# Kernel optimization log

Hardware: AMD Instinct MI355X
Metric: run time of the kernel (lower is better)

The kernel has to match this reference:

```python
import jax, jax.numpy as jnp
import numpy as np

N_SAMPLE = 32
BETA = 1.0


def setup_inputs() -> dict:
    key = jax.random.key(0)
    k1, k2 = jax.random.split(key)
    # small scales so the gaussian kernel over 512 dims does not underflow
    x = jax.random.normal(k1, (2048, 512), dtype=jnp.float32) * 0.05
    W = jax.random.normal(k2, (512, 2048), dtype=jnp.float32) * 0.02  # Dense kernel [in, hidden]
    return {"x": x, "W": W}


def reference(x, W):
    B, H = x.shape[0], W.shape[1]
    # Encoder: h = x W ; z = softmax(h * beita)
    h = x @ W                                   # [B, H]
    z = jax.nn.softmax(h * BETA, axis=-1)       # [B, H]
    # Sampler: tf.random.categorical treats z (probs) as LOGITS -> same here.
    key = jax.random.key(42)
    # tf gives [B, n_sample]; jax categorical with shape=(NS, B) then .T matches that,
    # and the original code then RESHAPES (not transposes) to [NS, B] -> replicate scramble.
    samp = jax.random.categorical(key, z, axis=-1, shape=(N_SAMPLE, B)).T  # [B, NS]
    samp = samp.reshape(N_SAMPLE, B)            # faithful reshape, not transpose
    onehot = jax.nn.one_hot(samp, H, dtype=x.dtype)          # [NS, B, H]
    # tensordot(onehot, W, axes=[2,1]) -> gather rows of W^T as dense matmul
    x_decoded = jnp.einsum('nbh,dh->nbd', onehot, W)          # [NS, B, D]
    # gauss(x[None], x_decoded), var=1
    diff = x[None, :, :] - x_decoded                          # [NS, B, D]
    coeff = 1.0 / jnp.sqrt(2.0 * jnp.pi)
    temp = coeff * jnp.exp(-0.5 * jnp.sum(diff * diff, axis=-1))  # [NS, B]
    weight = temp / jnp.mean(temp, axis=0)                    # broadcast over NS
    return (h, z, onehot, x_decoded, weight)
```

## Files before the change

### kernel.cpp

```cpp
#include <hip/hip_runtime.h>
#include <stdint.h>
#include <math.h>

static constexpr int BDIM = 2048;
static constexpr int HDIM = 2048;
static constexpr int DDIM = 512;
static constexpr int NSAMP = 32;

static constexpr size_t OFF_H  = 0;
static constexpr size_t OFF_Z  = (size_t)BDIM * HDIM;
static constexpr size_t OFF_OH = OFF_Z + (size_t)BDIM * HDIM;
static constexpr size_t OFF_XD = OFF_OH + (size_t)NSAMP * BDIM * HDIM;
static constexpr size_t OFF_W  = OFF_XD + (size_t)NSAMP * BDIM * DDIM;

static constexpr size_t WS_WT    = 0;
static constexpr size_t WS_XB    = 1048576;
static constexpr size_t WS_WTB   = WS_XB + 524288;
static constexpr size_t WS_SAMP  = WS_WTB + 524288;
static constexpr size_t WS_TEMP  = WS_SAMP + 65536;
static constexpr size_t WS_DELTA = WS_TEMP + 65536;

typedef __attribute__((ext_vector_type(8))) short short8;
typedef __attribute__((ext_vector_type(4))) float f32x4;

__device__ __forceinline__ ushort f2bf(float f) {
  uint32_t x = __float_as_uint(f);
  return (ushort)((x + 0x7FFFu + ((x >> 16) & 1u)) >> 16);
}

__global__ __launch_bounds__(256) void cast_x_kernel(const float* __restrict__ x,
                                                     ushort* __restrict__ xb) {
  const int i = (blockIdx.x * 256 + threadIdx.x) * 4;
  float4 v = *(const float4*)(x + i);
  ushort4 o = {f2bf(v.x), f2bf(v.y), f2bf(v.z), f2bf(v.w)};
  *(ushort4*)(xb + i) = o;
}

__global__ __launch_bounds__(256) void transpose_kernel(const float* __restrict__ W,
                                                        float* __restrict__ Wt,
                                                        ushort* __restrict__ Wtb) {
  __shared__ float tile[32][33];
  const int tx = threadIdx.x & 31, ty = threadIdx.x >> 5;
  const int bx = blockIdx.x;
  const int by = blockIdx.y;
#pragma unroll
  for (int i = 0; i < 32; i += 8)
    tile[ty + i][tx] = W[(size_t)(by * 32 + ty + i) * HDIM + bx * 32 + tx];
  __syncthreads();
#pragma unroll
  for (int i = 0; i < 32; i += 8) {
    float v = tile[tx][ty + i];
    const size_t o = (size_t)(bx * 32 + ty + i) * DDIM + by * 32 + tx;
    Wt[o] = v;
    Wtb[o] = f2bf(v);
  }
}

__global__ __launch_bounds__(256) void gemm_mfma_kernel(const ushort* __restrict__ xb,
                                                        const ushort* __restrict__ wtb,
                                                        float* __restrict__ h) {
  __shared__ short As[128][72];
  __shared__ short Bs[128][72];
  const int tid = threadIdx.x;
  const int bm = blockIdx.y * 128, bn = blockIdx.x * 128;
  const int wave = tid >> 6, lane = tid & 63;
  const int wm = (wave >> 1) * 64, wn = (wave & 1) * 64;
  const int lrow = lane & 15, lk = (lane >> 4) * 8;

  f32x4 acc[4][4] = {};

  const int srow = tid >> 3;
  const int scol = (tid & 7) * 8;

  for (int k0 = 0; k0 < DDIM; k0 += 64) {
#pragma unroll
    for (int p = 0; p < 4; ++p) {
      const int r = srow + p * 32;
      short8 av = *(const short8*)(xb + (size_t)(bm + r) * DDIM + k0 + scol);
      short8 bv = *(const short8*)(wtb + (size_t)(bn + r) * DDIM + k0 + scol);
      *(short8*)&As[r][scol] = av;
      *(short8*)&Bs[r][scol] = bv;
    }
    __syncthreads();
#pragma unroll
    for (int kk = 0; kk < 64; kk += 32) {
      short8 af[4], bf[4];
#pragma unroll
      for (int i = 0; i < 4; ++i) {
        af[i] = *(const short8*)&As[wm + i * 16 + lrow][kk + lk];
        bf[i] = *(const short8*)&Bs[wn + i * 16 + lrow][kk + lk];
      }
#pragma unroll
      for (int i = 0; i < 4; ++i)
#pragma unroll
        for (int j = 0; j < 4; ++j)
          acc[i][j] = __builtin_amdgcn_mfma_f32_16x16x32_bf16(af[i], bf[j], acc[i][j], 0, 0, 0);
    }
    __syncthreads();
  }
#pragma unroll
  for (int i = 0; i < 4; ++i)
#pragma unroll
    for (int j = 0; j < 4; ++j)
#pragma unroll
      for (int rg = 0; rg < 4; ++rg) {
        const int row = bm + wm + i * 16 + (lane >> 4) * 4 + rg;
        const int col = bn + wn + j * 16 + (lane & 15);
        h[(size_t)row * HDIM + col] = acc[i][j][rg];
      }
}

__global__ __launch_bounds__(256) void softmax_kernel(const float* __restrict__ h,
                                                      float* __restrict__ z,
                                                      float* __restrict__ rowDelta) {
  const int b = blockIdx.x;
  const int tid = threadIdx.x;
  const int lane = tid & 63, wav = tid >> 6;
  const float* row = h + (size_t)b * HDIM;
  float* zrow = z + (size_t)b * HDIM;
  __shared__ float wmaxs[4], wmins[4], wsums[4];

  float vals[8];
  float vmax = -INFINITY, vmin = INFINITY;
#pragma unroll
  for (int k = 0; k < 8; ++k) {
    float v = row[tid + (k << 8)];
    vals[k] = v;
    vmax = fmaxf(vmax, v);
    vmin = fminf(vmin, v);
  }
#pragma unroll
  for (int off = 32; off > 0; off >>= 1) {
    vmax = fmaxf(vmax, __shfl_xor(vmax, off, 64));
    vmin = fminf(vmin, __shfl_xor(vmin, off, 64));
  }
  if (lane == 0) { wmaxs[wav] = vmax; wmins[wav] = vmin; }
  __syncthreads();
  const float rmax = fmaxf(fmaxf(wmaxs[0], wmaxs[1]), fmaxf(wmaxs[2], wmaxs[3]));
  const float rmin = fminf(fminf(wmins[0], wmins[1]), fminf(wmins[2], wmins[3]));

  float e[8];
  float lsum = 0.f;
#pragma unroll
  for (int k = 0; k < 8; ++k) {
    e[k] = expf(vals[k] - rmax);
    lsum += e[k];
  }
#pragma unroll
  for (int off = 32; off > 0; off >>= 1) lsum += __shfl_xor(lsum, off, 64);
  if (lane == 0) wsums[wav] = lsum;
  __syncthreads();
  const float rsum = wsums[0] + wsums[1] + wsums[2] + wsums[3];
#pragma unroll
  for (int k = 0; k < 8; ++k) zrow[tid + (k << 8)] = e[k] / rsum;
  if (tid == 0) rowDelta[b] = (1.0f - expf(rmin - rmax)) / rsum;
}

__device__ __forceinline__ void threefry_0_42(uint32_t x0, uint32_t x1,
                                              uint32_t& o0, uint32_t& o1) {
  const uint32_t ks0 = 0u, ks1 = 42u, ks2 = 0x1BD11BDAu ^ 0u ^ 42u;
  x0 += ks0; x1 += ks1;
#define TF_R(r) { x0 += x1; x1 = (x1 << (r)) | (x1 >> (32 - (r))); x1 ^= x0; }
  TF_R(13) TF_R(15) TF_R(26) TF_R(6)   x0 += ks1; x1 += ks2 + 1u;
  TF_R(17) TF_R(29) TF_R(16) TF_R(24)  x0 += ks2; x1 += ks0 + 2u;
  TF_R(13) TF_R(15) TF_R(26) TF_R(6)   x0 += ks0; x1 += ks1 + 3u;
  TF_R(17) TF_R(29) TF_R(16) TF_R(24)  x0 += ks1; x1 += ks2 + 4u;
  TF_R(13) TF_R(15) TF_R(26) TF_R(6)   x0 += ks2; x1 += ks0 + 5u;
#undef TF_R
  o0 = x0; o1 = x1;
}

__device__ __forceinline__ float bits_to_u(uint32_t bits) {
  float f = __uint_as_float((bits >> 9) | 0x3f800000u) - 1.0f;
  return (f == 0.0f) ? 1.1754943508222875e-38f : f;
}

__global__ __launch_bounds__(256) void sample_kernel(const float* __restrict__ z,
                                                     const float* __restrict__ rowDelta,
                                                     int* __restrict__ samp) {
  const int wav = threadIdx.x >> 6;
  const int lane = threadIdx.x & 63;
  const int r = blockIdx.x * 4 + wav;
  const int b = r & (BDIM - 1);
  const float* zrow = z + (size_t)b * HDIM;

  const uint32_t base = (uint32_t)r << 11;
  uint32_t bb[32];
  uint32_t m23 = 0u;
#pragma unroll
  for (int k = 0; k < 32; ++k) {
    uint32_t o0, o1;
    threefry_0_42(0u, base + (uint32_t)(lane + (k << 6)), o0, o1);
    bb[k] = (o0 ^ o1) >> 9;
    m23 = max(m23, bb[k]);
  }
#pragma unroll
  for (int off = 32; off > 0; off >>= 1)
    m23 = max(m23, (uint32_t)__shfl_xor((int)m23, off, 64));
  const float umax = bits_to_u(m23 << 9);

  const float dpad = rowDelta[b] + 3e-4f;
  float uthr = expf(-expf(-(-logf(-logf(umax)) - dpad)));
  uthr = __uint_as_float(__float_as_uint(uthr) - 4u);
  uint32_t thr23 = __float_as_uint(1.0f + uthr) & 0x7FFFFFu;
  if (thr23 > 0u) thr23 -= 1u;

  double best = -1e300; int bh = 0x7fffffff;
#pragma unroll
  for (int k = 0; k < 32; ++k) {
    if (bb[k] >= thr23 || bb[k] == m23) {
      const int hh = lane + (k << 6);
      const float uk = bits_to_u(bb[k] << 9);
      double s = -log(-log((double)uk)) + (double)zrow[hh];
      if (s > best || (s == best && hh < bh)) { best = s; bh = hh; }
    }
  }
#pragma unroll
  for (int off = 32; off > 0; off >>= 1) {
    double so = __shfl_down(best, off, 64);
    int ho = __shfl_down(bh, off, 64);
    if (so > best || (so == best && ho < bh)) { best = so; bh = ho; }
  }
  if (lane == 0) samp[r] = bh;
}

__device__ __forceinline__ int scrambled_samp(const int* samp, int j) {
  return samp[((j & 31) << 11) | (j >> 5)];
}

__global__ __launch_bounds__(256) void onehot_scatter_kernel(const int* __restrict__ samp,
                                                             float* __restrict__ oh) {
  const int j = blockIdx.x * 256 + threadIdx.x;
  const int s = scrambled_samp(samp, j);
  oh[(size_t)j * HDIM + s] = 1.0f;
}

__global__ __launch_bounds__(256) void xdec_kernel(const float* __restrict__ x,
                                                   const float* __restrict__ Wt,
                                                   const int* __restrict__ samp,
                                                   float* __restrict__ xd,
                                                   float* __restrict__ temp) {
  const int j = blockIdx.x * 2 + (threadIdx.x >> 7);
  const int t = threadIdx.x & 127;
  const int s = scrambled_samp(samp, j);
  const int c = j & (BDIM - 1);

  const float4 wv = ((const float4*)(Wt + (size_t)s * DDIM))[t];
  const float4 xv = ((const float4*)(x + (size_t)c * DDIM))[t];
  ((float4*)(xd + (size_t)j * DDIM))[t] = wv;

  const float dx = xv.x - wv.x, dy = xv.y - wv.y, dz = xv.z - wv.z, dw = xv.w - wv.w;
  float ss = dx * dx + dy * dy + dz * dz + dw * dw;

  __shared__ float sred[256];
  sred[threadIdx.x] = ss;
  __syncthreads();
  for (int st = 64; st > 0; st >>= 1) {
    if (t < st) sred[threadIdx.x] += sred[threadIdx.x + st];
    __syncthreads();
  }
  if (t == 0) temp[j] = 0.3989422804014327f * expf(-0.5f * sred[threadIdx.x]);
}

__global__ __launch_bounds__(256) void weight_kernel(const float* __restrict__ temp,
                                                     float* __restrict__ wout) {
  const int c = blockIdx.x * 256 + threadIdx.x;
  if (c >= BDIM) return;
  float sum = 0.f;
#pragma unroll
  for (int a = 0; a < NSAMP; ++a) sum += temp[a * BDIM + c];
  const float mean = sum / 32.0f;
#pragma unroll
  for (int a = 0; a < NSAMP; ++a) wout[a * BDIM + c] = temp[a * BDIM + c] / mean;
}

extern "C" void kernel_launch(void* const* d_in, const int* in_sizes, int n_in,
                              void* d_out, int out_size, void* d_ws, size_t ws_size,
                              hipStream_t stream) {
  (void)in_sizes; (void)n_in; (void)out_size; (void)ws_size;
  const float* x = (const float*)d_in[0];
  const float* W = (const float*)d_in[1];
  float* out = (float*)d_out;

  float* h  = out + OFF_H;
  float* z  = out + OFF_Z;
  float* oh = out + OFF_OH;
  float* xd = out + OFF_XD;
  float* wo = out + OFF_W;

  float* ws = (float*)d_ws;
  float* Wt = ws + WS_WT;
  ushort* xb = (ushort*)(ws + WS_XB);
  ushort* Wtb = (ushort*)(ws + WS_WTB);
  int* samp = (int*)(ws + WS_SAMP);
  float* temp = ws + WS_TEMP;
  float* rowDelta = ws + WS_DELTA;

  hipMemsetAsync(oh, 0, (size_t)NSAMP * BDIM * HDIM * sizeof(float), stream);

  cast_x_kernel<<<1024, 256, 0, stream>>>(x, xb);
  transpose_kernel<<<dim3(64, 16), 256, 0, stream>>>(W, Wt, Wtb);
  gemm_mfma_kernel<<<dim3(16, 16), 256, 0, stream>>>(xb, Wtb, h);
  softmax_kernel<<<2048, 256, 0, stream>>>(h, z, rowDelta);
  sample_kernel<<<16384, 256, 0, stream>>>(z, rowDelta, samp);
  onehot_scatter_kernel<<<256, 256, 0, stream>>>(samp, oh);
  xdec_kernel<<<32768, 256, 0, stream>>>(x, Wt, samp, xd, temp);
  weight_kernel<<<8, 256, 0, stream>>>(temp, wo);
}
```

Measured before the change: 979.3 us.

## Fuse sampling, one-hot row write and decode into one kernel, drop memset

Sampling now writes each sampled row of the one-hot output directly, with full float4 rows of zeros and a single one, instead of a separate memset followed by a scatter. The same kernel also gathers the W row, writes x_decoded and computes the gaussian term with a wave shuffle reduction. This removes the intermediate samp buffer and two kernel launches. The shuffle was switched to xor so all lanes hold the argmax. Each sample wave now does more work, which may reduce the overlap of the RNG compute with the large store stream.

```diff
diff --git a/kernel.cpp b/kernel.cpp
--- a/kernel.cpp
+++ b/kernel.cpp
@@ -16,8 +16,7 @@
 static constexpr size_t WS_WT    = 0;
 static constexpr size_t WS_XB    = 1048576;
 static constexpr size_t WS_WTB   = WS_XB + 524288;
-static constexpr size_t WS_SAMP  = WS_WTB + 524288;
-static constexpr size_t WS_TEMP  = WS_SAMP + 65536;
+static constexpr size_t WS_TEMP  = WS_WTB + 524288;
 static constexpr size_t WS_DELTA = WS_TEMP + 65536;
 
 typedef __attribute__((ext_vector_type(8))) short short8;
@@ -175,9 +174,10 @@
   return (f == 0.0f) ? 1.1754943508222875e-38f : f;
 }
 
-__global__ __launch_bounds__(256) void sample_kernel(const float* __restrict__ z,
-                                                     const float* __restrict__ rowDelta,
-                                                     int* __restrict__ samp) {
+__global__ __launch_bounds__(256) void sample_fused_kernel(
+    const float* __restrict__ z, const float* __restrict__ rowDelta,
+    const float* __restrict__ x, const float* __restrict__ Wt,
+    float* __restrict__ oh, float* __restrict__ xd, float* __restrict__ temp) {
   const int wav = threadIdx.x >> 6;
   const int lane = threadIdx.x & 63;
   const int r = blockIdx.x * 4 + wav;
@@ -217,49 +217,44 @@
   }
 #pragma unroll
   for (int off = 32; off > 0; off >>= 1) {
-    double so = __shfl_down(best, off, 64);
-    int ho = __shfl_down(bh, off, 64);
+    double so = __shfl_xor(best, off, 64);
+    int ho = __shfl_xor(bh, off, 64);
     if (so > best || (so == best && ho < bh)) { best = so; bh = ho; }
   }
-  if (lane == 0) samp[r] = bh;
-}
-
-__device__ __forceinline__ int scrambled_samp(const int* samp, int j) {
-  return samp[((j & 31) << 11) | (j >> 5)];
-}
-
-__global__ __launch_bounds__(256) void onehot_scatter_kernel(const int* __restrict__ samp,
-                                                             float* __restrict__ oh) {
-  const int j = blockIdx.x * 256 + threadIdx.x;
-  const int s = scrambled_samp(samp, j);
-  oh[(size_t)j * HDIM + s] = 1.0f;
-}
-
-__global__ __launch_bounds__(256) void xdec_kernel(const float* __restrict__ x,
-                                                   const float* __restrict__ Wt,
-                                                   const int* __restrict__ samp,
-                                                   float* __restrict__ xd,
-                                                   float* __restrict__ temp) {
-  const int j = blockIdx.x * 2 + (threadIdx.x >> 7);
-  const int t = threadIdx.x & 127;
-  const int s = scrambled_samp(samp, j);
+
+  const int j = ((r & (BDIM - 1)) << 5) | (r >> 11);
   const int c = j & (BDIM - 1);
 
-  const float4 wv = ((const float4*)(Wt + (size_t)s * DDIM))[t];
-  const float4 xv = ((const float4*)(x + (size_t)c * DDIM))[t];
-  ((float4*)(xd + (size_t)j * DDIM))[t] = wv;
-
-  const float dx = xv.x - wv.x, dy = xv.y - wv.y, dz = xv.z - wv.z, dw = xv.w - wv.w;
-  float ss = dx * dx + dy * dy + dz * dz + dw * dw;
-
-  __shared__ float sred[256];
-  sred[threadIdx.x] = ss;
-  __syncthreads();
-  for (int st = 64; st > 0; st >>= 1) {
-    if (t < st) sred[threadIdx.x] += sred[threadIdx.x + st];
-    __syncthreads();
-  }
-  if (t == 0) temp[j] = 0.3989422804014327f * expf(-0.5f * sred[threadIdx.x]);
+  float* ohrow = oh + (size_t)j * HDIM;
+#pragma unroll
+  for (int k = 0; k < 8; ++k) {
+    const int idx4 = (k << 6) + lane;
+    const unsigned d = (unsigned)(bh - (idx4 << 2));
+    float4 v;
+    v.x = (d == 0u) ? 1.f : 0.f;
+    v.y = (d == 1u) ? 1.f : 0.f;
+    v.z = (d == 2u) ? 1.f : 0.f;
+    v.w = (d == 3u) ? 1.f : 0.f;
+    ((float4*)ohrow)[idx4] = v;
+  }
+
+  const float4* wrow = (const float4*)(Wt + (size_t)bh * DDIM);
+  const float4* xrow = (const float4*)(x + (size_t)c * DDIM);
+  float4* xdrow = (float4*)(xd + (size_t)j * DDIM);
+  float ss = 0.f;
+#pragma unroll
+  for (int k = 0; k < 2; ++k) {
+    const int idx4 = (k << 6) + lane;
+    const float4 wv = wrow[idx4];
+    const float4 xv = xrow[idx4];
+    xdrow[idx4] = wv;
+    const float dx = xv.x - wv.x, dy = xv.y - wv.y;
+    const float dz = xv.z - wv.z, dw = xv.w - wv.w;
+    ss += dx * dx + dy * dy + dz * dz + dw * dw;
+  }
+#pragma unroll
+  for (int off = 32; off > 0; off >>= 1) ss += __shfl_xor(ss, off, 64);
+  if (lane == 0) temp[j] = 0.3989422804014327f * expf(-0.5f * ss);
 }
 
 __global__ __launch_bounds__(256) void weight_kernel(const float* __restrict__ temp,
@@ -292,18 +287,13 @@
   float* Wt = ws + WS_WT;
   ushort* xb = (ushort*)(ws + WS_XB);
   ushort* Wtb = (ushort*)(ws + WS_WTB);
-  int* samp = (int*)(ws + WS_SAMP);
   float* temp = ws + WS_TEMP;
   float* rowDelta = ws + WS_DELTA;
-
-  hipMemsetAsync(oh, 0, (size_t)NSAMP * BDIM * HDIM * sizeof(float), stream);
 
   cast_x_kernel<<<1024, 256, 0, stream>>>(x, xb);
   transpose_kernel<<<dim3(64, 16), 256, 0, stream>>>(W, Wt, Wtb);
   gemm_mfma_kernel<<<dim3(16, 16), 256, 0, stream>>>(xb, Wtb, h);
   softmax_kernel<<<2048, 256, 0, stream>>>(h, z, rowDelta);
-  sample_kernel<<<16384, 256, 0, stream>>>(z, rowDelta, samp);
-  onehot_scatter_kernel<<<256, 256, 0, stream>>>(samp, oh);
-  xdec_kernel<<<32768, 256, 0, stream>>>(x, Wt, samp, xd, temp);
+  sample_fused_kernel<<<16384, 256, 0, stream>>>(z, rowDelta, x, Wt, oh, xd, temp);
   weight_kernel<<<8, 256, 0, stream>>>(temp, wo);
 }
```

Measured after the change: 871.4 us. -11.0%, faster.
